# Performance work log

Hardware: AMD Instinct MI355X
Metric: run time of the kernel (lower is better)

The kernel has to match this reference:

```python
import jax, jax.numpy as jnp
import numpy as np

B, N, F_IN, F_OUT = 8, 2048, 128, 64
ALPHA = 0.2  # LeakyReLU negative slope
NEG_BIG = -9e15


def setup_inputs() -> dict:
    key = jax.random.key(0)
    k1, k2, k3, k4 = jax.random.split(key, 4)
    x = jax.random.normal(k1, (B, N, F_IN), dtype=jnp.float32)
    adj = jax.random.randint(k2, (B, N, N), 0, 2, dtype=jnp.int32)
    # xavier-uniform-ish init scale for faithfulness (gain=1.414)
    w_lim = 1.414 * np.sqrt(6.0 / (F_IN + F_OUT))
    a_lim = 1.414 * np.sqrt(6.0 / (2 * F_OUT + 1))
    weight = jax.random.uniform(k3, (F_IN, F_OUT), minval=-w_lim, maxval=w_lim, dtype=jnp.float32)
    weight2 = jax.random.uniform(k4, (2 * F_OUT, 1), minval=-a_lim, maxval=a_lim, dtype=jnp.float32)
    return {"x": x, "adj": adj, "weight": weight, "weight2": weight2}


def reference(x, adj, weight, weight2):
    # Linear projection: [B, N, F_out]
    wh = jnp.einsum("bnf,fo->bno", x, weight)
    # Additive GAT decomposition of concat-score:
    # e_ij = leakyrelu(a1 . Wh_i + a2 . Wh_j)  == original concat @ weight2
    a1 = weight2[:F_OUT, 0]   # [F_out]
    a2 = weight2[F_OUT:, 0]   # [F_out]
    s1 = wh @ a1              # [B, N]
    s2 = wh @ a2              # [B, N]
    e = s1[:, :, None] + s2[:, None, :]          # [B, N, N]
    e = jnp.where(e > 0, e, ALPHA * e)            # LeakyReLU
    e = jnp.where(adj > 0, e, NEG_BIG)            # mask non-edges
    attention = jax.nn.softmax(e, axis=2)         # [B, N, N]
    # dropout is identity in eval mode (training=False)
    out = jnp.einsum("bij,bjo->bio", attention, wh)  # [B, N, F_out]
    return jax.nn.elu(out)
```

## Files before the change

### kernel.cpp

```cpp
#include <hip/hip_runtime.h>
#include <cstdint>
#include <cstddef>

#define B_    8
#define N_    2048
#define FIN   128
#define FOUT  64
#define ALPHA 0.2f
#define LOG2E 1.4426950408889634f

typedef __attribute__((ext_vector_type(8))) _Float16 half8;
typedef __attribute__((ext_vector_type(4))) _Float16 half4;
typedef __attribute__((ext_vector_type(4))) float float4v;

__global__ __launch_bounds__(256) void k0_convW(
    const float* __restrict__ W, _Float16* __restrict__ WtG)
{
    int o = blockIdx.x * 256 + threadIdx.x;
    int f = o >> 7, k = o & 127;
    float v = W[k * FOUT + f];
    _Float16 hi = (_Float16)v;
    _Float16 lo = (_Float16)(v - (float)hi);
    WtG[o] = hi;
    WtG[FOUT * FIN + o] = lo;
}

__global__ __launch_bounds__(256) void kp_pack(
    const int* __restrict__ adj, unsigned long long* __restrict__ maskp)
{
    int t = threadIdx.x, lane = t & 63, w = t >> 6;
    size_t row = (size_t)blockIdx.x * 4 + w;
    const int* rp = adj + row * N_ + lane;
    unsigned long long* orow = maskp + row * 32;

    int a[32];
    #pragma unroll
    for (int it = 0; it < 32; ++it) a[it] = rp[it * 64];
    #pragma unroll
    for (int it = 0; it < 32; ++it) {
        unsigned long long m = __ballot(a[it] > 0);
        if (lane == 0) orow[it] = m;
    }
}

__global__ __launch_bounds__(256, 2) void k1_wh(
    const float* __restrict__ x, const _Float16* __restrict__ WtG,
    const float* __restrict__ w2, _Float16* __restrict__ whT,
    float* __restrict__ s1, float* __restrict__ s2)
{
    __shared__ __attribute__((aligned(16))) _Float16 xth[32][136];
    __shared__ __attribute__((aligned(16))) _Float16 xtl[32][136];
    __shared__ float s1p[4][32];
    __shared__ float s2p[4][32];

    int t = threadIdx.x, lane = t & 63, w = t >> 6;
    int b = blockIdx.x >> 6;
    int r0 = (blockIdx.x & 63) << 5;
    const float* xb = x + ((size_t)b * N_ + r0) * FIN;

    #pragma unroll
    for (int j = 0; j < 4; ++j) {
        int idx = t + j * 256;
        int row = idx >> 5;
        int k0 = (idx & 31) * 4;
        float4 v = ((const float4*)xb)[idx];
        float vv[4] = {v.x, v.y, v.z, v.w};
        half4 h, l;
        #pragma unroll
        for (int e = 0; e < 4; ++e) {
            _Float16 hi = (_Float16)vv[e];
            h[e] = hi;
            l[e] = (_Float16)(vv[e] - (float)hi);
        }
        *(half4*)&xth[row][k0] = h;
        *(half4*)&xtl[row][k0] = l;
    }
    __syncthreads();

    int l15 = lane & 15, quad = lane >> 4;
    int f0 = w * 16;

    half8 bh[4], bl[4];
    const _Float16* wgh = WtG + (f0 + l15) * FIN + quad * 8;
    #pragma unroll
    for (int c = 0; c < 4; ++c) {
        bh[c] = *(const half8*)(wgh + c * 32);
        bl[c] = *(const half8*)(wgh + FOUT * FIN + c * 32);
    }
    float a1f = w2[f0 + l15], a2f = w2[FOUT + f0 + l15];

    #pragma unroll
    for (int rt = 0; rt < 2; ++rt) {
        float4v acc = {0.f, 0.f, 0.f, 0.f};
        #pragma unroll
        for (int c = 0; c < 4; ++c) {
            half8 ah = *(const half8*)&xth[rt * 16 + l15][c * 32 + quad * 8];
            half8 al = *(const half8*)&xtl[rt * 16 + l15][c * 32 + quad * 8];
            acc = __builtin_amdgcn_mfma_f32_16x16x32_f16(ah, bh[c], acc, 0, 0, 0);
            acc = __builtin_amdgcn_mfma_f32_16x16x32_f16(ah, bl[c], acc, 0, 0, 0);
            acc = __builtin_amdgcn_mfma_f32_16x16x32_f16(al, bh[c], acc, 0, 0, 0);
        }
        half4 hv;
        #pragma unroll
        for (int reg = 0; reg < 4; ++reg) hv[reg] = (_Float16)acc[reg];
        *(half4*)(whT + ((size_t)b * FOUT + f0 + l15) * N_ + r0 + rt * 16 + quad * 4) = hv;

        #pragma unroll
        for (int reg = 0; reg < 4; ++reg) {
            float v1 = acc[reg] * a1f;
            float v2 = acc[reg] * a2f;
            #pragma unroll
            for (int m = 1; m <= 8; m <<= 1) {
                v1 += __shfl_xor(v1, m);
                v2 += __shfl_xor(v2, m);
            }
            if (l15 == 0) {
                s1p[w][rt * 16 + quad * 4 + reg] = v1;
                s2p[w][rt * 16 + quad * 4 + reg] = v2;
            }
        }
    }
    __syncthreads();
    if (t < 32) {
        float v = s1p[0][t] + s1p[1][t] + s1p[2][t] + s1p[3][t];
        s1[(size_t)b * N_ + r0 + t] = v;
    } else if (t < 64) {
        int r = t - 32;
        float v = s2p[0][r] + s2p[1][r] + s2p[2][r] + s2p[3][r];
        s2[(size_t)b * N_ + r0 + r] = v;
    }
}

__global__ __launch_bounds__(256, 4) void k2_attn(
    const unsigned* __restrict__ mask32, const _Float16* __restrict__ whT,
    const float* __restrict__ s1, const float* __restrict__ s2,
    float* __restrict__ out)
{
    __shared__ __attribute__((aligned(16))) _Float16 pT[2][16][264];
    __shared__ float lL[16];
    __shared__ float smaxL[4];

    int t = threadIdx.x, lane = t & 63, w = t >> 6;
    int b = blockIdx.x >> 7;
    int i0 = (blockIdx.x & 127) << 4;

    const float4* s2v = (const float4*)(s2 + (size_t)b * N_);
    float4 ua_ = s2v[t], ub_ = s2v[t + 256];
    float vm = fmaxf(fmaxf(fmaxf(ua_.x, ua_.y), fmaxf(ua_.z, ua_.w)),
                     fmaxf(fmaxf(ub_.x, ub_.y), fmaxf(ub_.z, ub_.w)));
    #pragma unroll
    for (int m = 32; m >= 1; m >>= 1) vm = fmaxf(vm, __shfl_xor(vm, m));
    if (lane == 0) smaxL[w] = vm;
    __syncthreads();
    float s2max = fmaxf(fmaxf(smaxL[0], smaxL[1]), fmaxf(smaxL[2], smaxL[3]));

    int l15 = lane & 15, quad = lane >> 4;
    int f0 = w * 16;
    int shn = (lane & 7) * 4;

    float c1[4], c2[4], lacc[4];
    #pragma unroll
    for (int rr = 0; rr < 4; ++rr) {
        float sv = s1[(size_t)b * N_ + i0 + w * 4 + rr];
        float mm = sv + s2max;
        float mh = fmaxf(mm, ALPHA * mm);
        c1[rr] = (sv - mh) * LOG2E;
        c2[rr] = (ALPHA * sv - mh) * LOG2E;
        lacc[rr] = 0.f;
    }

    const unsigned* mB = mask32 + ((size_t)b * N_ + i0 + w * 4) * 64 + (lane >> 3);
    const float* s2L = s2 + (size_t)b * N_ + lane * 4;

    float4v acc = {0.f, 0.f, 0.f, 0.f};
    const _Float16* wB = whT + ((size_t)b * FOUT + f0 + l15) * N_ + quad * 8;

    #pragma unroll 1
    for (int c = 0; c < 8; ++c) {
        unsigned mbits[4];
        #pragma unroll
        for (int rr = 0; rr < 4; ++rr)
            mbits[rr] = (mB[(size_t)rr * 64 + c * 8] >> shn) & 0xFu;
        float4 sv = *(const float4*)(s2L + c * 256);
        half8 bfr[8];
        const _Float16* wp = wB + c * 256;
        #pragma unroll
        for (int kk = 0; kk < 8; ++kk) bfr[kk] = *(const half8*)(wp + kk * 32);

        float u[4]  = {sv.x * LOG2E, sv.y * LOG2E, sv.z * LOG2E, sv.w * LOG2E};
        float ua[4] = {u[0] * ALPHA, u[1] * ALPHA, u[2] * ALPHA, u[3] * ALPHA};
        #pragma unroll
        for (int rr = 0; rr < 4; ++rr) {
            int r = w * 4 + rr;
            half4 pf;
            float ls = 0.f;
            #pragma unroll
            for (int e = 0; e < 4; ++e) {
                float tt = fmaxf(c1[rr] + u[e], c2[rr] + ua[e]);
#if __has_builtin(__builtin_amdgcn_exp2f)
                float p = __builtin_amdgcn_exp2f(tt);
#else
                float p = exp2f(tt);
#endif
                p = (mbits[rr] & (1u << e)) ? p : 0.f;
                ls += p;
                pf[e] = (_Float16)p;
            }
            lacc[rr] += ls;
            *(half4*)&pT[c & 1][r][lane * 4] = pf;
        }

        if (c == 7) {
            #pragma unroll
            for (int rr = 0; rr < 4; ++rr) {
                float v = lacc[rr];
                #pragma unroll
                for (int m = 32; m >= 1; m >>= 1) v += __shfl_xor(v, m);
                if (lane == 0) lL[w * 4 + rr] = v;
            }
        }

        __syncthreads();

        #pragma unroll
        for (int kk = 0; kk < 8; ++kk) {
            half8 af = *(const half8*)&pT[c & 1][l15][kk * 32 + quad * 8];
            acc = __builtin_amdgcn_mfma_f32_16x16x32_f16(af, bfr[kk], acc, 0, 0, 0);
        }
    }

    #pragma unroll
    for (int reg = 0; reg < 4; ++reg) {
        int row = quad * 4 + reg;
        float val = acc[reg] / lL[row];
        val = (val > 0.f) ? val : (__expf(val) - 1.f);
        out[((size_t)b * N_ + i0 + row) * FOUT + f0 + l15] = val;
    }
}

extern "C" void kernel_launch(void* const* d_in, const int* in_sizes, int n_in,
                              void* d_out, int out_size, void* d_ws, size_t ws_size,
                              hipStream_t stream) {
    const float* x   = (const float*)d_in[0];
    const int*   adj = (const int*)d_in[1];
    const float* W   = (const float*)d_in[2];
    const float* w2  = (const float*)d_in[3];
    float* out = (float*)d_out;

    char* ws = (char*)d_ws;
    _Float16* whT = (_Float16*)ws;
    float* s1  = (float*)(ws + 2097152);
    float* s2  = (float*)(ws + 2097152 + 65536);
    _Float16* WtG = (_Float16*)(ws + 2097152 + 131072);
    unsigned long long* maskp =
        (unsigned long long*)(ws + 2097152 + 131072 + 32768);

    k0_convW<<<32, 256, 0, stream>>>(W, WtG);
    kp_pack<<<(B_ * N_) / 4, 256, 0, stream>>>(adj, maskp);
    k1_wh<<<(B_ * N_) / 32, 256, 0, stream>>>(x, WtG, w2, whT, s1, s2);
    k2_attn<<<(B_ * N_) / 16, 256, 0, stream>>>((const unsigned*)maskp, whT, s1, s2, out);
}
```

Baseline: 239.9 us.

## Fuse weight conversion and adjacency bit-packing into projection kernel; prefetch attention loop

```diff
diff --git a/kernel.cpp b/kernel.cpp
--- a/kernel.cpp
+++ b/kernel.cpp
@@ -13,40 +13,11 @@
 typedef __attribute__((ext_vector_type(4))) _Float16 half4;
 typedef __attribute__((ext_vector_type(4))) float float4v;
 
-__global__ __launch_bounds__(256) void k0_convW(
-    const float* __restrict__ W, _Float16* __restrict__ WtG)
-{
-    int o = blockIdx.x * 256 + threadIdx.x;
-    int f = o >> 7, k = o & 127;
-    float v = W[k * FOUT + f];
-    _Float16 hi = (_Float16)v;
-    _Float16 lo = (_Float16)(v - (float)hi);
-    WtG[o] = hi;
-    WtG[FOUT * FIN + o] = lo;
-}
-
-__global__ __launch_bounds__(256) void kp_pack(
-    const int* __restrict__ adj, unsigned long long* __restrict__ maskp)
-{
-    int t = threadIdx.x, lane = t & 63, w = t >> 6;
-    size_t row = (size_t)blockIdx.x * 4 + w;
-    const int* rp = adj + row * N_ + lane;
-    unsigned long long* orow = maskp + row * 32;
-
-    int a[32];
-    #pragma unroll
-    for (int it = 0; it < 32; ++it) a[it] = rp[it * 64];
-    #pragma unroll
-    for (int it = 0; it < 32; ++it) {
-        unsigned long long m = __ballot(a[it] > 0);
-        if (lane == 0) orow[it] = m;
-    }
-}
-
 __global__ __launch_bounds__(256, 2) void k1_wh(
-    const float* __restrict__ x, const _Float16* __restrict__ WtG,
-    const float* __restrict__ w2, _Float16* __restrict__ whT,
-    float* __restrict__ s1, float* __restrict__ s2)
+    const float* __restrict__ x, const float* __restrict__ W,
+    const float* __restrict__ w2, const int* __restrict__ adj,
+    _Float16* __restrict__ whT, float* __restrict__ s1, float* __restrict__ s2,
+    unsigned long long* __restrict__ maskp)
 {
     __shared__ __attribute__((aligned(16))) _Float16 xth[32][136];
     __shared__ __attribute__((aligned(16))) _Float16 xtl[32][136];
@@ -81,11 +52,16 @@
     int f0 = w * 16;
 
     half8 bh[4], bl[4];
-    const _Float16* wgh = WtG + (f0 + l15) * FIN + quad * 8;
+    const float* wcol = W + (f0 + l15);
     #pragma unroll
     for (int c = 0; c < 4; ++c) {
-        bh[c] = *(const half8*)(wgh + c * 32);
-        bl[c] = *(const half8*)(wgh + FOUT * FIN + c * 32);
+        #pragma unroll
+        for (int e = 0; e < 8; ++e) {
+            float v = wcol[(size_t)(c * 32 + quad * 8 + e) * FOUT];
+            _Float16 hi = (_Float16)v;
+            bh[c][e] = hi;
+            bl[c][e] = (_Float16)(v - (float)hi);
+        }
     }
     float a1f = w2[f0 + l15], a2f = w2[FOUT + f0 + l15];
 
@@ -129,6 +105,21 @@
         float v = s2p[0][r] + s2p[1][r] + s2p[2][r] + s2p[3][r];
         s2[(size_t)b * N_ + r0 + r] = v;
     }
+
+    size_t growbase = (size_t)b * N_ + r0 + (size_t)w * 8;
+    #pragma unroll 1
+    for (int r = 0; r < 8; ++r) {
+        const int* rp = adj + (growbase + r) * N_ + lane;
+        unsigned long long* orow = maskp + (growbase + r) * 32;
+        int a[32];
+        #pragma unroll
+        for (int it = 0; it < 32; ++it) a[it] = rp[it * 64];
+        #pragma unroll
+        for (int it = 0; it < 32; ++it) {
+            unsigned long long m = __ballot(a[it] > 0);
+            if (lane == 0) orow[it] = m;
+        }
+    }
 }
 
 __global__ __launch_bounds__(256, 4) void k2_attn(
@@ -171,46 +162,70 @@
 
     const unsigned* mB = mask32 + ((size_t)b * N_ + i0 + w * 4) * 64 + (lane >> 3);
     const float* s2L = s2 + (size_t)b * N_ + lane * 4;
+    const _Float16* wB = whT + ((size_t)b * FOUT + f0 + l15) * N_ + quad * 8;
 
     float4v acc = {0.f, 0.f, 0.f, 0.f};
-    const _Float16* wB = whT + ((size_t)b * FOUT + f0 + l15) * N_ + quad * 8;
+
+    unsigned mb0[4], mb1[4];
+    float4 sv0, sv1;
+    half8 bfr[8];
+
+#define LOADMS(cc, MB, SV) do {                                              \
+        _Pragma("unroll")                                                    \
+        for (int rr_ = 0; rr_ < 4; ++rr_)                                    \
+            MB[rr_] = mB[(size_t)rr_ * 64 + (cc) * 8];                       \
+        SV = *(const float4*)(s2L + (cc) * 256);                             \
+    } while (0)
+
+#define LOADBF(cc) do {                                                      \
+        const _Float16* wp_ = wB + (cc) * 256;                               \
+        _Pragma("unroll")                                                    \
+        for (int kk_ = 0; kk_ < 8; ++kk_)                                    \
+            bfr[kk_] = *(const half8*)(wp_ + kk_ * 32);                      \
+    } while (0)
+
+#define PCOMP(MB, SV, PB) do {                                               \
+        float u_[4]  = {SV.x * LOG2E, SV.y * LOG2E, SV.z * LOG2E, SV.w * LOG2E}; \
+        float ua2_[4] = {u_[0] * ALPHA, u_[1] * ALPHA, u_[2] * ALPHA, u_[3] * ALPHA}; \
+        _Pragma("unroll")                                                    \
+        for (int rr_ = 0; rr_ < 4; ++rr_) {                                  \
+            unsigned mbits_ = (MB[rr_] >> shn) & 0xFu;                       \
+            half4 pf_;                                                       \
+            float ls_ = 0.f;                                                 \
+            _Pragma("unroll")                                                \
+            for (int e_ = 0; e_ < 4; ++e_) {                                 \
+                float tt_ = fmaxf(c1[rr_] + u_[e_], c2[rr_] + ua2_[e_]);     \
+                float p_ = __builtin_amdgcn_exp2f(tt_);                      \
+                p_ = (mbits_ & (1u << e_)) ? p_ : 0.f;                       \
+                ls_ += p_;                                                   \
+                pf_[e_] = (_Float16)p_;                                      \
+            }                                                                \
+            lacc[rr_] += ls_;                                                \
+            *(half4*)&pT[PB][w * 4 + rr_][lane * 4] = pf_;                   \
+        }                                                                    \
+    } while (0)
+
+#define MFMA8(PB) do {                                                       \
+        _Pragma("unroll")                                                    \
+        for (int kk_ = 0; kk_ < 8; ++kk_) {                                  \
+            half8 af_ = *(const half8*)&pT[PB][l15][kk_ * 32 + quad * 8];    \
+            acc = __builtin_amdgcn_mfma_f32_16x16x32_f16(af_, bfr[kk_], acc, 0, 0, 0); \
+        }                                                                    \
+    } while (0)
+
+    LOADMS(0, mb0, sv0);
 
     #pragma unroll 1
-    for (int c = 0; c < 8; ++c) {
-        unsigned mbits[4];
-        #pragma unroll
-        for (int rr = 0; rr < 4; ++rr)
-            mbits[rr] = (mB[(size_t)rr * 64 + c * 8] >> shn) & 0xFu;
-        float4 sv = *(const float4*)(s2L + c * 256);
-        half8 bfr[8];
-        const _Float16* wp = wB + c * 256;
-        #pragma unroll
-        for (int kk = 0; kk < 8; ++kk) bfr[kk] = *(const half8*)(wp + kk * 32);
-
-        float u[4]  = {sv.x * LOG2E, sv.y * LOG2E, sv.z * LOG2E, sv.w * LOG2E};
-        float ua[4] = {u[0] * ALPHA, u[1] * ALPHA, u[2] * ALPHA, u[3] * ALPHA};
-        #pragma unroll
-        for (int rr = 0; rr < 4; ++rr) {
-            int r = w * 4 + rr;
-            half4 pf;
-            float ls = 0.f;
-            #pragma unroll
-            for (int e = 0; e < 4; ++e) {
-                float tt = fmaxf(c1[rr] + u[e], c2[rr] + ua[e]);
-#if __has_builtin(__builtin_amdgcn_exp2f)
-                float p = __builtin_amdgcn_exp2f(tt);
-#else
-                float p = exp2f(tt);
-#endif
-                p = (mbits[rr] & (1u << e)) ? p : 0.f;
-                ls += p;
-                pf[e] = (_Float16)p;
-            }
-            lacc[rr] += ls;
-            *(half4*)&pT[c & 1][r][lane * 4] = pf;
-        }
-
-        if (c == 7) {
+    for (int c = 0; c < 8; c += 2) {
+        LOADBF(c);
+        LOADMS(c + 1, mb1, sv1);
+        PCOMP(mb0, sv0, 0);
+        __syncthreads();
+        MFMA8(0);
+        LOADBF(c + 1);
+        if (c < 6) LOADMS(c + 2, mb0, sv0);
+        PCOMP(mb1, sv1, 1);
+        if (c == 6) {
             #pragma unroll
             for (int rr = 0; rr < 4; ++rr) {
                 float v = lacc[rr];
@@ -219,15 +234,13 @@
                 if (lane == 0) lL[w * 4 + rr] = v;
             }
         }
-
         __syncthreads();
-
-        #pragma unroll
-        for (int kk = 0; kk < 8; ++kk) {
-            half8 af = *(const half8*)&pT[c & 1][l15][kk * 32 + quad * 8];
-            acc = __builtin_amdgcn_mfma_f32_16x16x32_f16(af, bfr[kk], acc, 0, 0, 0);
-        }
-    }
+        MFMA8(1);
+    }
+#undef LOADMS
+#undef LOADBF
+#undef PCOMP
+#undef MFMA8
 
     #pragma unroll
     for (int reg = 0; reg < 4; ++reg) {
@@ -251,12 +264,9 @@
     _Float16* whT = (_Float16*)ws;
     float* s1  = (float*)(ws + 2097152);
     float* s2  = (float*)(ws + 2097152 + 65536);
-    _Float16* WtG = (_Float16*)(ws + 2097152 + 131072);
     unsigned long long* maskp =
-        (unsigned long long*)(ws + 2097152 + 131072 + 32768);
-
-    k0_convW<<<32, 256, 0, stream>>>(W, WtG);
-    kp_pack<<<(B_ * N_) / 4, 256, 0, stream>>>(adj, maskp);
-    k1_wh<<<(B_ * N_) / 32, 256, 0, stream>>>(x, WtG, w2, whT, s1, s2);
+        (unsigned long long*)(ws + 2097152 + 131072);
+
+    k1_wh<<<(B_ * N_) / 32, 256, 0, stream>>>(x, W, w2, adj, whT, s1, s2, maskp);
     k2_attn<<<(B_ * N_) / 16, 256, 0, stream>>>((const unsigned*)maskp, whT, s1, s2, out);
 }
```

Result: no change. 241.2 us (+0.6%).
